# Kernel tuning notes

Hardware: AMD Instinct MI355X
Metric: run time of the kernel (lower is better)

Reference implementation:

```python
import jax, jax.numpy as jnp
import numpy as np

N_FFT = 2048
HOP = 512
WIN = 2048
PAD = N_FFT // 2  # center padding, n_fft // 2


def setup_inputs() -> dict:
    key = jax.random.key(0)
    x = jax.random.normal(key, (16, 262144), dtype=jnp.float32)
    # periodic Hann window, identical to torch.hann_window(2048)
    window = (0.5 - 0.5 * jnp.cos(2.0 * jnp.pi * jnp.arange(WIN) / WIN)).astype(jnp.float32)
    return {"x": x, "window": window}


def reference(x, window):
    # x: [B, T]; center reflect-pad by n_fft//2 on both sides (matches F.pad mode='reflect')
    xp = jnp.pad(x, ((0, 0), (PAD, PAD)), mode="reflect")
    n_frames = (xp.shape[-1] - N_FFT) // HOP + 1  # static
    # strided framing (replaces the identity-conv im2col in the original)
    idx = jnp.arange(n_frames)[:, None] * HOP + jnp.arange(N_FFT)[None, :]  # [F, n_fft]
    frames = xp[:, idx] * window  # [B, F, n_fft], windowed frames
    # windowed DFT; rfft of windowed frame == F.linear(frames, fft_k) in the original
    spec = jnp.fft.rfft(frames, axis=-1)  # [B, F, n_fft//2+1] complex
    real = jnp.real(spec).transpose(0, 2, 1)  # [B, dim, F]
    imag = jnp.imag(spec).transpose(0, 2, 1)  # [B, dim, F]
    return (real, imag)
```

## Files before the change

kernel.cpp:

```cpp
#include <hip/hip_runtime.h>


#define N_FFT   2048
#define LOG2N   11
#define HOP     512
#define PADL    1024
#define NBINS   1025
#define NFRAMES 513
#define NBATCH  16
#define TLEN    262144

#define HALF_OUT ((size_t)NBATCH * NBINS * NFRAMES)

__device__ __forceinline__ int pidx(int a) { return a + (a >> 5); }

__device__ __forceinline__ int refl(int j) {
    if (j < 0)          j = -j;
    else if (j >= TLEN) j = 2 * TLEN - 2 - j;
    return j;
}

__device__ __forceinline__ float2 cmul(float2 a, float2 w) {
    return make_float2(fmaf(a.x, w.x, -a.y * w.y), fmaf(a.x, w.y, a.y * w.x));
}
__device__ __forceinline__ float2 cadd(float2 a, float2 b) {
    return make_float2(a.x + b.x, a.y + b.y);
}
__device__ __forceinline__ float2 csub(float2 a, float2 b) {
    return make_float2(a.x - b.x, a.y - b.y);
}
__device__ __forceinline__ float2 csqr(float2 w) {
    return make_float2(fmaf(w.x, w.x, -w.y * w.y), 2.0f * w.x * w.y);
}

template <int H, int L2H>
__device__ __forceinline__ void octet_pass(float2* __restrict__ zc, int q) {
    const int p    = q & (H - 1);
    const int base = ((q >> L2H) << (L2H + 3)) + p;
    int ia[8];
#pragma unroll
    for (int m = 0; m < 8; ++m) ia[m] = pidx(base + m * H);
    float2 v0 = zc[ia[0]], v1 = zc[ia[1]], v2 = zc[ia[2]], v3 = zc[ia[3]];
    float2 v4 = zc[ia[4]], v5 = zc[ia[5]], v6 = zc[ia[6]], v7 = zc[ia[7]];

    float2 w1, w2, w3;
    if (H == 1) {
        w3 = make_float2(1.0f, 0.0f); w2 = w3; w1 = w3;
    } else {
        float s, c;
        __sincosf((float)p * (-3.14159265358979323846f / (4.0f * (float)H)), &s, &c);
        w3 = make_float2(c, s);
        w2 = csqr(w3);
        w1 = csqr(w2);
    }

    float2 t;
    t = cmul(v1, w1); v1 = csub(v0, t); v0 = cadd(v0, t);
    t = cmul(v3, w1); v3 = csub(v2, t); v2 = cadd(v2, t);
    t = cmul(v5, w1); v5 = csub(v4, t); v4 = cadd(v4, t);
    t = cmul(v7, w1); v7 = csub(v6, t); v6 = cadd(v6, t);
    const float2 w2m = make_float2(w2.y, -w2.x);
    t = cmul(v2, w2);  v2 = csub(v0, t); v0 = cadd(v0, t);
    t = cmul(v3, w2m); v3 = csub(v1, t); v1 = cadd(v1, t);
    t = cmul(v6, w2);  v6 = csub(v4, t); v4 = cadd(v4, t);
    t = cmul(v7, w2m); v7 = csub(v5, t); v5 = cadd(v5, t);
    const float R = 0.70710678118654752f;
    const float2 w3o  = make_float2((w3.x + w3.y) * R, (w3.y - w3.x) * R);
    const float2 w3m  = make_float2(w3.y, -w3.x);
    const float2 w3mo = make_float2(w3o.y, -w3o.x);
    t = cmul(v4, w3);   v4 = csub(v0, t); v0 = cadd(v0, t);
    t = cmul(v5, w3o);  v5 = csub(v1, t); v1 = cadd(v1, t);
    t = cmul(v6, w3m);  v6 = csub(v2, t); v2 = cadd(v2, t);
    t = cmul(v7, w3mo); v7 = csub(v3, t); v3 = cadd(v3, t);

    zc[ia[0]] = v0; zc[ia[1]] = v1; zc[ia[2]] = v2; zc[ia[3]] = v3;
    zc[ia[4]] = v4; zc[ia[5]] = v5; zc[ia[6]] = v6; zc[ia[7]] = v7;
}

__global__ __launch_bounds__(1024) void stft_one(
    const float* __restrict__ x,
    const float* __restrict__ window,
    float* __restrict__ out)
{
    __shared__ float2 z[9][2112];

    const int d     = blockIdx.x + 32 * blockIdx.y;
    const int pair  = (d >> 4) * 8 + (d & 7);
    const int gg    = 2 * pair + ((d >> 3) & 1);
    const int b     = gg >> 5;
    const int g     = gg & 31;
    const int tid   = threadIdx.x;
    const int f0    = g * 16;
    const int nsub  = (g == 31) ? 9 : 8;

    const float* xb = x + (size_t)b * TLEN;
    for (int idx = tid; idx < nsub * 2048; idx += 1024) {
        const int c  = idx >> 11;
        const int n  = idx & 2047;
        const int fa = f0 + 2 * c;
        const float w  = window[n];
        const float va = xb[refl(fa * HOP - PADL + n)] * w;
        const float vb = xb[refl((fa + 1) * HOP - PADL + n)] * w;
        const int r = (int)(__brev((unsigned)n) >> (32 - LOG2N));
        z[c][pidx(r)] = make_float2(va, vb);
    }
    __syncthreads();

    for (int idx = tid; idx < nsub * 256; idx += 1024)
        octet_pass<1, 0>(z[idx >> 8], idx & 255);
    __syncthreads();
    for (int idx = tid; idx < nsub * 256; idx += 1024)
        octet_pass<8, 3>(z[idx >> 8], idx & 255);
    __syncthreads();
    for (int idx = tid; idx < nsub * 256; idx += 1024)
        octet_pass<64, 6>(z[idx >> 8], idx & 255);
    __syncthreads();

    for (int idx = tid; idx < nsub * 512; idx += 1024) {
        const int c = idx >> 9;
        const int p = idx & 511;
        float s, cc;
        __sincosf((float)p * (-3.14159265358979323846f / 1024.0f), &s, &cc);
        const float2 w2  = make_float2(cc, s);
        const float2 w1  = csqr(w2);
        const float2 w2m = make_float2(w2.y, -w2.x);
        const int i0 = pidx(p), i1 = pidx(p + 512), i2 = pidx(p + 1024), i3 = pidx(p + 1536);
        float2 v0 = z[c][i0], v1 = z[c][i1], v2 = z[c][i2], v3 = z[c][i3];
        float2 t;
        t = cmul(v1, w1); v1 = csub(v0, t); v0 = cadd(v0, t);
        t = cmul(v3, w1); v3 = csub(v2, t); v2 = cadd(v2, t);
        t = cmul(v2, w2);  v2 = csub(v0, t); v0 = cadd(v0, t);
        t = cmul(v3, w2m); v3 = csub(v1, t); v1 = cadd(v1, t);
        z[c][i0] = v0; z[c][i1] = v1; z[c][i2] = v2; z[c][i3] = v3;
    }
    __syncthreads();

    float* __restrict__ outr = out;
    float* __restrict__ outi = out + HALF_OUT;
    for (int k = tid; k < NBINS; k += 1024) {
        const int km = (N_FFT - k) & (N_FFT - 1);
        const size_t orow = ((size_t)b * NBINS + (size_t)k) * NFRAMES + (size_t)f0;
#pragma unroll
        for (int c = 0; c < 8; ++c) {
            const float2 zk = z[c][pidx(k)];
            const float2 zr = z[c][pidx(km)];
            outr[orow + 2 * c]     = 0.5f * (zk.x + zr.x);
            outr[orow + 2 * c + 1] = 0.5f * (zk.y + zr.y);
            outi[orow + 2 * c]     = 0.5f * (zk.y - zr.y);
            outi[orow + 2 * c + 1] = 0.5f * (zr.x - zk.x);
        }
        if (nsub == 9) {
            const float2 zk = z[8][pidx(k)];
            const float2 zr = z[8][pidx(km)];
            outr[orow + 16] = 0.5f * (zk.x + zr.x);
            outi[orow + 16] = 0.5f * (zk.y - zr.y);
        }
    }
}

extern "C" void kernel_launch(void* const* d_in, const int* in_sizes, int n_in,
                              void* d_out, int out_size, void* d_ws, size_t ws_size,
                              hipStream_t stream) {
    const float* x      = (const float*)d_in[0];
    const float* window = (const float*)d_in[1];
    float* out          = (float*)d_out;

    dim3 grid(32, NBATCH);
    stft_one<<<grid, 1024, 0, stream>>>(x, window, out);
}
```

Measured before the change: 127.3 us.

## Split work into smaller 512-thread blocks of 8 frames for better occupancy

Each block now handles 8 frames (4 packed complex FFTs) with 512 threads instead of 16-17 frames with 1024 threads, and the grid grows from 512 to 1040 blocks. The last frame gets its own 16 tail blocks, and blocks are remapped so neighbouring tiles stay on the same XCD. Each block uses much less LDS, so more blocks can share a CU and more work can run at once. The output store loop is reorganised so each thread writes 4 consecutive frames. The cost is more blocks and a separate pass for the tail frame.

```diff
diff --git a/kernel.cpp b/kernel.cpp
--- a/kernel.cpp
+++ b/kernel.cpp
@@ -77,24 +77,32 @@
     zc[ia[4]] = v4; zc[ia[5]] = v5; zc[ia[6]] = v6; zc[ia[7]] = v7;
 }
 
-__global__ __launch_bounds__(1024) void stft_one(
+__global__ __launch_bounds__(512, 4) void stft_one(
     const float* __restrict__ x,
     const float* __restrict__ window,
     float* __restrict__ out)
 {
-    __shared__ float2 z[9][2112];
+    __shared__ float2 z[4][2113];
 
-    const int d     = blockIdx.x + 32 * blockIdx.y;
-    const int pair  = (d >> 4) * 8 + (d & 7);
-    const int gg    = 2 * pair + ((d >> 3) & 1);
-    const int b     = gg >> 5;
-    const int g     = gg & 31;
-    const int tid   = threadIdx.x;
-    const int f0    = g * 16;
-    const int nsub  = (g == 31) ? 9 : 8;
+    const int d = blockIdx.x;
+    int b, g;
+    if (d >= 1024) {
+        b = d - 1024;
+        g = 64;
+    } else {
+        const int xcd  = d & 7;
+        const int slot = d >> 3;
+        const int Q    = (slot >> 2) * 8 + xcd;
+        const int L    = Q * 4 + (slot & 3);
+        b = L >> 6;
+        g = L & 63;
+    }
+    const int tid = threadIdx.x;
+    const int f0  = g * 8;
+    const int npl = (g == 64) ? 1 : 4;
 
     const float* xb = x + (size_t)b * TLEN;
-    for (int idx = tid; idx < nsub * 2048; idx += 1024) {
+    for (int idx = tid; idx < npl * 2048; idx += 512) {
         const int c  = idx >> 11;
         const int n  = idx & 2047;
         const int fa = f0 + 2 * c;
@@ -106,17 +114,17 @@
     }
     __syncthreads();
 
-    for (int idx = tid; idx < nsub * 256; idx += 1024)
+    for (int idx = tid; idx < npl * 256; idx += 512)
         octet_pass<1, 0>(z[idx >> 8], idx & 255);
     __syncthreads();
-    for (int idx = tid; idx < nsub * 256; idx += 1024)
+    for (int idx = tid; idx < npl * 256; idx += 512)
         octet_pass<8, 3>(z[idx >> 8], idx & 255);
     __syncthreads();
-    for (int idx = tid; idx < nsub * 256; idx += 1024)
+    for (int idx = tid; idx < npl * 256; idx += 512)
         octet_pass<64, 6>(z[idx >> 8], idx & 255);
     __syncthreads();
 
-    for (int idx = tid; idx < nsub * 512; idx += 1024) {
+    for (int idx = tid; idx < npl * 512; idx += 512) {
         const int c = idx >> 9;
         const int p = idx & 511;
         float s, cc;
@@ -137,23 +145,34 @@
 
     float* __restrict__ outr = out;
     float* __restrict__ outi = out + HALF_OUT;
-    for (int k = tid; k < NBINS; k += 1024) {
-        const int km = (N_FFT - k) & (N_FFT - 1);
-        const size_t orow = ((size_t)b * NBINS + (size_t)k) * NFRAMES + (size_t)f0;
-#pragma unroll
-        for (int c = 0; c < 8; ++c) {
-            const float2 zk = z[c][pidx(k)];
-            const float2 zr = z[c][pidx(km)];
-            outr[orow + 2 * c]     = 0.5f * (zk.x + zr.x);
-            outr[orow + 2 * c + 1] = 0.5f * (zk.y + zr.y);
-            outi[orow + 2 * c]     = 0.5f * (zk.y - zr.y);
-            outi[orow + 2 * c + 1] = 0.5f * (zr.x - zk.x);
+    if (g < 64) {
+        for (int idx = tid; idx < 2 * NBINS; idx += 512) {
+            const int k  = idx >> 1;
+            const int h  = idx & 1;
+            const int km = (N_FFT - k) & (N_FFT - 1);
+            const float2 zk0 = z[2 * h][pidx(k)];
+            const float2 zr0 = z[2 * h][pidx(km)];
+            const float2 zk1 = z[2 * h + 1][pidx(k)];
+            const float2 zr1 = z[2 * h + 1][pidx(km)];
+            const size_t o = ((size_t)b * NBINS + (size_t)k) * NFRAMES
+                           + (size_t)(f0 + 4 * h);
+            outr[o + 0] = 0.5f * (zk0.x + zr0.x);
+            outr[o + 1] = 0.5f * (zk0.y + zr0.y);
+            outr[o + 2] = 0.5f * (zk1.x + zr1.x);
+            outr[o + 3] = 0.5f * (zk1.y + zr1.y);
+            outi[o + 0] = 0.5f * (zk0.y - zr0.y);
+            outi[o + 1] = 0.5f * (zr0.x - zk0.x);
+            outi[o + 2] = 0.5f * (zk1.y - zr1.y);
+            outi[o + 3] = 0.5f * (zr1.x - zk1.x);
         }
-        if (nsub == 9) {
-            const float2 zk = z[8][pidx(k)];
-            const float2 zr = z[8][pidx(km)];
-            outr[orow + 16] = 0.5f * (zk.x + zr.x);
-            outi[orow + 16] = 0.5f * (zk.y - zr.y);
+    } else {
+        for (int k = tid; k < NBINS; k += 512) {
+            const int km = (N_FFT - k) & (N_FFT - 1);
+            const float2 zk = z[0][pidx(k)];
+            const float2 zr = z[0][pidx(km)];
+            const size_t o = ((size_t)b * NBINS + (size_t)k) * NFRAMES + 512;
+            outr[o] = 0.5f * (zk.x + zr.x);
+            outi[o] = 0.5f * (zk.y - zr.y);
         }
     }
 }
@@ -165,6 +184,6 @@
     const float* window = (const float*)d_in[1];
     float* out          = (float*)d_out;
 
-    dim3 grid(32, NBATCH);
-    stft_one<<<grid, 1024, 0, stream>>>(x, window, out);
+    dim3 grid(1040);
+    stft_one<<<grid, 512, 0, stream>>>(x, window, out);
 }
```

After: 113.4 us. 1.12x faster.
